# Performance work log

Hardware: AMD Instinct MI355X
Metric: run time of the kernel (lower is better)

The kernel has to match this reference:

```python
import jax, jax.numpy as jnp
import numpy as np


def setup_inputs() -> dict:
    key = jax.random.key(0)
    ks = jax.random.split(key, 5)
    B, Cin, Ch, H, W, K = 8, 64, 64, 128, 128, 3
    fan_in = (Cin + Ch) * K * K
    return {
        "x": jax.random.normal(ks[0], (B, Cin, H, W), jnp.float32),
        "prev_h": jax.random.normal(ks[1], (B, Ch, H, W), jnp.float32),
        "prev_c": jax.random.normal(ks[2], (B, Ch, H, W), jnp.float32),
        "W_gates": jax.random.normal(ks[3], (4 * Ch, Cin + Ch, K, K), jnp.float32) / np.sqrt(fan_in),
        "b_gates": jax.random.normal(ks[4], (4 * Ch,), jnp.float32) * 0.01,
    }


def reference(x, prev_h, prev_c, W_gates, b_gates):
    # ConvLSTM cell: conv over concat(input, prev_h) -> 4 gates -> gating.
    pad = W_gates.shape[-1] // 2
    stacked = jnp.concatenate([x, prev_h], axis=1)  # [B, Cin+Ch, H, W]
    gates = jax.lax.conv_general_dilated(
        stacked, W_gates,
        window_strides=(1, 1),
        padding=[(pad, pad), (pad, pad)],
        dimension_numbers=("NCHW", "OIHW", "NCHW"),
    ) + b_gates[None, :, None, None]  # [B, 4*Ch, H, W]
    in_gate, remember_gate, out_gate, cell_gate = jnp.split(gates, 4, axis=1)
    in_gate = jax.nn.sigmoid(in_gate)
    remember_gate = jax.nn.sigmoid(remember_gate)
    out_gate = jax.nn.sigmoid(out_gate)
    cell_gate = jnp.tanh(cell_gate)
    cell = in_gate * cell_gate + remember_gate * prev_c
    hidden = out_gate * jnp.tanh(cell)
    return (hidden, cell)
```

## Files before the change

### kernel.cpp

```cpp
#include <hip/hip_runtime.h>

typedef __attribute__((ext_vector_type(8))) short short8;
typedef __attribute__((ext_vector_type(16))) float float16;

#define NPIX_HID 8388608

__device__ __forceinline__ short f2bf(float f) {
    union { float f; unsigned u; } v; v.f = f;
    unsigned r = (v.u + 0x7FFFu + ((v.u >> 16) & 1u)) >> 16;
    return (short)r;
}

__device__ __forceinline__ float sigmoidf_(float v) { return 1.f / (1.f + __expf(-v)); }
__device__ __forceinline__ float tanhf_(float v)    { return 2.f / (1.f + __expf(-2.f * v)) - 1.f; }

__global__ void wprep(const float* __restrict__ W, short* __restrict__ A) {
    int tid = blockIdx.x * 256 + threadIdx.x;
    if (tid >= 9 * 16 * 8 * 32 * 8) return;
    int j   = tid & 7;
    int r   = (tid >> 3) & 31;
    int t   = (tid >> 8) & 7;
    int cig = (tid >> 11) & 15;
    int kk  = tid >> 15;
    int g = r >> 3, cl = r & 7;
    int co = g * 64 + t * 8 + cl;
    int ci = cig * 8 + j;
    A[tid] = f2bf(W[co * 1152 + ci * 9 + kk]);
}

__global__ __launch_bounds__(256, 2) void convlstm_main(
    const float* __restrict__ x, const float* __restrict__ ph,
    const float* __restrict__ pc, const short* __restrict__ aprep,
    const float* __restrict__ bg, float* __restrict__ out)
{
    __shared__ short Bs[4 * 66 * 128];

    const int tid  = threadIdx.x;
    const int lane = tid & 63;
    const int wave = tid >> 6;
    const int l31  = lane & 31;
    const int h    = lane >> 5;
    const int mhalf = wave & 1;
    const int nhalf = wave >> 1;

    const int t  = blockIdx.x;
    const int x0 = (t & 1) * 64;
    const int y0 = ((t >> 1) & 63) * 2;
    const int b  = t >> 7;

    for (int i = tid; i < 4224; i += 256) {
        const int px  = i % 66;
        const int ro  = i / 66;
        const int oct = ro & 15;
        const int row = ro >> 4;
        const int ysrc = y0 + row - 1;
        const int xsrc = x0 + px - 1;
        short8 pk = {0,0,0,0,0,0,0,0};
        if ((unsigned)ysrc < 128u && (unsigned)xsrc < 128u) {
            const float* src = (oct < 8) ? x : ph;
            const float* sp = src + (((b * 64 + (oct & 7) * 8) * 128 + ysrc) * 128 + xsrc);
#pragma unroll
            for (int j = 0; j < 8; ++j) pk[j] = f2bf(sp[j * 16384]);
        }
        const int off16 = (row * 66 + px) * 16 + (oct ^ (px & 15));
        *(short8*)&Bs[off16 * 8] = pk;
    }
    __syncthreads();

    float16 acc[4][2];
#pragma unroll
    for (int mt = 0; mt < 4; ++mt)
#pragma unroll
        for (int nt = 0; nt < 2; ++nt)
#pragma unroll
            for (int e = 0; e < 16; ++e) acc[mt][nt][e] = 0.f;

    const short* ap0 = aprep + h * 2048 + l31 * 8 + mhalf * 1024;
    const short* ap1 = ap0 + 4096;

    short8 abuf[2][2][4];
#pragma unroll
    for (int ks = 0; ks < 2; ++ks)
#pragma unroll
        for (int mt = 0; mt < 4; ++mt)
            abuf[0][ks][mt] = *(const short8*)((ks ? ap1 : ap0) + mt * 256);

    const int lB = l31;

#define HALF_BODY(KT, P, ADV)                                                      \
    {                                                                              \
        const int kt  = (KT);                                                      \
        const int kkk = kt >> 2, kc = kt & 3;                                      \
        const int ky  = (kkk * 11) >> 5;                                           \
        const int kx  = kkk - ky * 3;                                              \
        if (ADV) { ap0 += 8192; ap1 += 8192;                                       \
            _Pragma("unroll")                                                      \
            for (int ks = 0; ks < 2; ++ks)                                         \
                _Pragma("unroll")                                                  \
                for (int mt = 0; mt < 4; ++mt)                                     \
                    abuf[(P) ^ 1][ks][mt] =                                        \
                        *(const short8*)((ks ? ap1 : ap0) + mt * 256);             \
        }                                                                          \
        const int pxb = kx + lB;                                                   \
        const int q   = pxb & 15;                                                  \
        const int rh  = ky + nhalf;                                                \
        short8 bfr[2][2];                                                          \
        _Pragma("unroll")                                                          \
        for (int ks = 0; ks < 2; ++ks) {                                           \
            const int gx = ((kc * 4 + ks * 2) | h) ^ q;                            \
            _Pragma("unroll")                                                      \
            for (int nt = 0; nt < 2; ++nt) {                                       \
                const int off16 = (rh * 66 + nt * 32 + pxb) * 16 + gx;             \
                bfr[ks][nt] = *(const short8*)&Bs[off16 * 8];                      \
            }                                                                      \
        }                                                                          \
        _Pragma("unroll")                                                          \
        for (int mt = 0; mt < 4; ++mt)                                             \
            _Pragma("unroll")                                                      \
            for (int nt = 0; nt < 2; ++nt) {                                       \
                acc[mt][nt] = __builtin_amdgcn_mfma_f32_32x32x16_bf16(             \
                    abuf[P][0][mt], bfr[0][nt], acc[mt][nt], 0, 0, 0);             \
                acc[mt][nt] = __builtin_amdgcn_mfma_f32_32x32x16_bf16(             \
                    abuf[P][1][mt], bfr[1][nt], acc[mt][nt], 0, 0, 0);             \
            }                                                                      \
    }

#pragma unroll 1
    for (int it = 0; it < 18; ++it) {
        const int kt0 = it * 2;
        HALF_BODY(kt0, 0, 1)
        HALF_BODY(kt0 + 1, 1, (it < 17))
    }
#undef HALF_BODY

    const int yy = y0 + nhalf;
#pragma unroll
    for (int mt = 0; mt < 4; ++mt) {
        const int c0 = (mhalf * 4 + mt) * 8 + 4 * h;
#pragma unroll
        for (int nt = 0; nt < 2; ++nt) {
            const int px = x0 + nt * 32 + l31;
#pragma unroll
            for (int a = 0; a < 4; ++a) {
                const int c = c0 + a;
                const float gi = acc[mt][nt][a]      + bg[c];
                const float gf = acc[mt][nt][4 + a]  + bg[64 + c];
                const float go = acc[mt][nt][8 + a]  + bg[128 + c];
                const float gc = acc[mt][nt][12 + a] + bg[192 + c];
                const float ig = sigmoidf_(gi);
                const float fg = sigmoidf_(gf);
                const float og = sigmoidf_(go);
                const float cg = tanhf_(gc);
                const int idx = ((b * 64 + c) * 128 + yy) * 128 + px;
                const float cell = ig * cg + fg * pc[idx];
                const float hid  = og * tanhf_(cell);
                out[idx] = hid;
                out[NPIX_HID + idx] = cell;
            }
        }
    }
}

extern "C" void kernel_launch(void* const* d_in, const int* in_sizes, int n_in,
                              void* d_out, int out_size, void* d_ws, size_t ws_size,
                              hipStream_t stream) {
    const float* x  = (const float*)d_in[0];
    const float* ph = (const float*)d_in[1];
    const float* pc = (const float*)d_in[2];
    const float* W  = (const float*)d_in[3];
    const float* bg = (const float*)d_in[4];
    float* out = (float*)d_out;
    short* aprep = (short*)d_ws;

    wprep<<<1152, 256, 0, stream>>>(W, aprep);
    convlstm_main<<<1024, 256, 0, stream>>>(x, ph, pc, aprep, bg, out);
}
```

Measured before the change: 235.0 us.

## Pre-convert inputs to bf16 pixel-major layout and tile conv by full rows

Adds a separate kernel that converts x and prev_h to bf16 in a pixel-major, channel-contiguous layout in workspace. The main kernel then copies contiguous 16-byte vectors into a padded shared-memory buffer instead of doing strided fp32 gathers with inline conversion. Each block now handles one full output row, processes the input channels in two 64-channel phases to keep shared memory small, and uses a matching reordered weight layout. The cost is an extra pass that writes and rereads a 32 MB intermediate plus an extra launch. The old path is kept as a fallback when the workspace is too small.

```diff
diff --git a/kernel.cpp b/kernel.cpp
--- a/kernel.cpp
+++ b/kernel.cpp
@@ -1,39 +1,59 @@
 #include <hip/hip_runtime.h>
 
 typedef __attribute__((ext_vector_type(8))) short short8;
+typedef __attribute__((ext_vector_type(4))) short short4v;
 typedef __attribute__((ext_vector_type(16))) float float16;
 
 #define NPIX_HID 8388608
+#define ROWU 1170
+#define ROWB 18720
+#define WS_NEED (589824u + 33554432u)
 
 __device__ __forceinline__ short f2bf(float f) {
     union { float f; unsigned u; } v; v.f = f;
     unsigned r = (v.u + 0x7FFFu + ((v.u >> 16) & 1u)) >> 16;
     return (short)r;
 }
-
 __device__ __forceinline__ float sigmoidf_(float v) { return 1.f / (1.f + __expf(-v)); }
 __device__ __forceinline__ float tanhf_(float v)    { return 2.f / (1.f + __expf(-2.f * v)) - 1.f; }
 
-__global__ void wprep(const float* __restrict__ W, short* __restrict__ A) {
+__global__ void wprep2(const float* __restrict__ W, short* __restrict__ A) {
     int tid = blockIdx.x * 256 + threadIdx.x;
-    if (tid >= 9 * 16 * 8 * 32 * 8) return;
-    int j   = tid & 7;
-    int r   = (tid >> 3) & 31;
-    int t   = (tid >> 8) & 7;
-    int cig = (tid >> 11) & 15;
-    int kk  = tid >> 15;
-    int g = r >> 3, cl = r & 7;
-    int co = g * 64 + t * 8 + cl;
-    int ci = cig * 8 + j;
-    A[tid] = f2bf(W[co * 1152 + ci * 9 + kk]);
-}
-
-__global__ __launch_bounds__(256, 2) void convlstm_main(
-    const float* __restrict__ x, const float* __restrict__ ph,
-    const float* __restrict__ pc, const short* __restrict__ aprep,
-    const float* __restrict__ bg, float* __restrict__ out)
+    if (tid >= 294912) return;
+    int j = tid & 7, r = (tid >> 3) & 31, t = (tid >> 8) & 7;
+    int h = (tid >> 11) & 1, s = (tid >> 12) & 3;
+    int ht = tid >> 14;
+    int half = ht / 9, tap = ht - half * 9;
+    int co = (r >> 3) * 64 + t * 8 + (r & 7);
+    int ci = half * 64 + s * 16 + h * 8 + j;
+    A[tid] = f2bf(W[co * 1152 + ci * 9 + tap]);
+}
+
+__global__ void bprep_k(const float* __restrict__ x, const float* __restrict__ ph,
+                        short* __restrict__ B) {
+    int tid = blockIdx.x * 256 + threadIdx.x;
+    int px = tid & 127;
+    int yy = (tid >> 7) & 127;
+    int half = (tid >> 14) & 1;
+    int bb = tid >> 15;
+    const float* src = half ? ph : x;
+    const float* sp = src + ((size_t)(bb * 64) * 128 + yy) * 128 + px;
+    short* dst = B + (size_t)(((bb * 128 + yy) * 2 + half)) * 8192 + px * 64;
+#pragma unroll
+    for (int oct = 0; oct < 8; ++oct) {
+        short8 pk;
+#pragma unroll
+        for (int j = 0; j < 8; ++j) pk[j] = f2bf(sp[(oct * 8 + j) * 16384]);
+        *(short8*)(dst + oct * 8) = pk;
+    }
+}
+
+__global__ __launch_bounds__(256, 2) void convlstm_mainB(
+    const short* __restrict__ bprep, const short* __restrict__ aprep,
+    const float* __restrict__ pc, const float* __restrict__ bg,
+    float* __restrict__ out)
 {
-    __shared__ short Bs[4 * 66 * 128];
+    __shared__ short Bs[3 * ROWU * 8];
 
     const int tid  = threadIdx.x;
     const int lane = tid & 63;
@@ -41,20 +61,170 @@
     const int l31  = lane & 31;
     const int h    = lane >> 5;
     const int mhalf = wave & 1;
-    const int nhalf = wave >> 1;
+    const int xhalf = wave >> 1;
 
     const int t  = blockIdx.x;
-    const int x0 = (t & 1) * 64;
-    const int y0 = ((t >> 1) & 63) * 2;
+    const int y0 = t & 127;
     const int b  = t >> 7;
 
+    float16 acc[4][2];
+#pragma unroll
+    for (int mt = 0; mt < 4; ++mt)
+#pragma unroll
+        for (int nt = 0; nt < 2; ++nt)
+#pragma unroll
+            for (int e = 0; e < 16; ++e) acc[mt][nt][e] = 0.f;
+
+    const short* apl = aprep + h * 2048 + mhalf * 1024 + l31 * 8;
+    short8 abuf[2][2][4];
+#pragma unroll
+    for (int ss = 0; ss < 2; ++ss)
+#pragma unroll
+        for (int mt = 0; mt < 4; ++mt)
+            abuf[0][ss][mt] = *(const short8*)(apl + ss * 4096 + mt * 256);
+    const short* apn = apl + 8192;
+
+    const int vb = ((xhalf * 64 + l31) * 9 + h) * 16;
+    char* bsb = (char*)Bs;
+
+#pragma unroll 1
+    for (int phse = 0; phse < 2; ++phse) {
+        if (phse) __syncthreads();
+        if (tid < 48) {
+            int r = tid >> 4, sd = (tid >> 3) & 1, oc = tid & 7;
+            short8 z = {0,0,0,0,0,0,0,0};
+            *(short8*)&Bs[(r * ROWU + sd * 129 * 9 + oc) * 8] = z;
+        }
+#pragma unroll 1
+        for (int r = 0; r < 3; ++r) {
+            int ysrc = y0 + r - 1;
+            if ((unsigned)ysrc < 128u) {
+                const short* gsrc = bprep + (size_t)(((b * 128 + ysrc) * 2 + phse)) * 8192;
+#pragma unroll
+                for (int c = 0; c < 4; ++c) {
+                    int k = c * 256 + tid;
+                    int px = k >> 3, oc = k & 7;
+                    short8 v = *(const short8*)(gsrc + k * 8);
+                    *(short8*)&Bs[(r * ROWU + (px + 1) * 9 + oc) * 8] = v;
+                }
+            } else {
+                short8 z = {0,0,0,0,0,0,0,0};
+#pragma unroll
+                for (int c = 0; c < 4; ++c) {
+                    int k = c * 256 + tid;
+                    int px = k >> 3, oc = k & 7;
+                    *(short8*)&Bs[(r * ROWU + (px + 1) * 9 + oc) * 8] = z;
+                }
+            }
+        }
+        __syncthreads();
+
+#pragma unroll 1
+        for (int q2 = 0; q2 < 9; ++q2) {
+            const int ky = q2 / 3;
+            const int kx = q2 - ky * 3;
+            const int ub = ky * ROWB + kx * 144;
+            {
+#pragma unroll
+                for (int ss = 0; ss < 2; ++ss)
+#pragma unroll
+                    for (int mt = 0; mt < 4; ++mt)
+                        abuf[1][ss][mt] = *(const short8*)(apn + ss * 4096 + mt * 256);
+                apn += 8192;
+#pragma unroll
+                for (int ss = 0; ss < 2; ++ss) {
+                    short8 bfr[2];
+#pragma unroll
+                    for (int nt = 0; nt < 2; ++nt)
+                        bfr[nt] = *(const short8*)(bsb + vb + (ub + nt * 4608 + ss * 32));
+#pragma unroll
+                    for (int mt = 0; mt < 4; ++mt)
+#pragma unroll
+                        for (int nt = 0; nt < 2; ++nt)
+                            acc[mt][nt] = __builtin_amdgcn_mfma_f32_32x32x16_bf16(
+                                abuf[0][ss][mt], bfr[nt], acc[mt][nt], 0, 0, 0);
+                }
+            }
+            {
+                if (!((phse == 1) && (q2 == 8))) {
+#pragma unroll
+                    for (int ss = 0; ss < 2; ++ss)
+#pragma unroll
+                        for (int mt = 0; mt < 4; ++mt)
+                            abuf[0][ss][mt] = *(const short8*)(apn + ss * 4096 + mt * 256);
+                    apn += 8192;
+                }
+#pragma unroll
+                for (int ss = 0; ss < 2; ++ss) {
+                    const int s = 2 + ss;
+                    short8 bfr[2];
+#pragma unroll
+                    for (int nt = 0; nt < 2; ++nt)
+                        bfr[nt] = *(const short8*)(bsb + vb + (ub + nt * 4608 + s * 32));
+#pragma unroll
+                    for (int mt = 0; mt < 4; ++mt)
+#pragma unroll
+                        for (int nt = 0; nt < 2; ++nt)
+                            acc[mt][nt] = __builtin_amdgcn_mfma_f32_32x32x16_bf16(
+                                abuf[1][ss][mt], bfr[nt], acc[mt][nt], 0, 0, 0);
+                }
+            }
+        }
+    }
+
+#pragma unroll
+    for (int mt = 0; mt < 4; ++mt) {
+        const int c0 = (mhalf * 4 + mt) * 8 + 4 * h;
+#pragma unroll
+        for (int nt = 0; nt < 2; ++nt) {
+            const int px = xhalf * 64 + nt * 32 + l31;
+#pragma unroll
+            for (int a = 0; a < 4; ++a) {
+                const int c = c0 + a;
+                const float gi = acc[mt][nt][a]      + bg[c];
+                const float gf = acc[mt][nt][4 + a]  + bg[64 + c];
+                const float go = acc[mt][nt][8 + a]  + bg[128 + c];
+                const float gc = acc[mt][nt][12 + a] + bg[192 + c];
+                const float ig = sigmoidf_(gi);
+                const float fg = sigmoidf_(gf);
+                const float og = sigmoidf_(go);
+                const float cg = tanhf_(gc);
+                const int idx = ((b * 64 + c) * 128 + y0) * 128 + px;
+                const float cell = ig * cg + fg * pc[idx];
+                const float hid  = og * tanhf_(cell);
+                out[idx] = hid;
+                out[NPIX_HID + idx] = cell;
+            }
+        }
+    }
+}
+
+__global__ void wprep5(const float* __restrict__ W, short* __restrict__ A) {
+    int tid = blockIdx.x * 256 + threadIdx.x;
+    if (tid >= 9 * 16 * 8 * 32 * 8) return;
+    int j = tid & 7, r = (tid >> 3) & 31, t = (tid >> 8) & 7;
+    int cig = (tid >> 11) & 15, kk = tid >> 15;
+    int g = r >> 3, cl = r & 7;
+    int co = g * 64 + t * 8 + cl;
+    int ci = cig * 8 + j;
+    A[tid] = f2bf(W[co * 1152 + ci * 9 + kk]);
+}
+
+__global__ __launch_bounds__(256, 2) void convlstm_main5(
+    const float* __restrict__ x, const float* __restrict__ ph,
+    const float* __restrict__ pc, const short* __restrict__ aprep,
+    const float* __restrict__ bg, float* __restrict__ out)
+{
+    __shared__ short Bs[4 * 66 * 128];
+    const int tid = threadIdx.x, lane = tid & 63, wave = tid >> 6;
+    const int l31 = lane & 31, h = lane >> 5;
+    const int mhalf = wave & 1, nhalf = wave >> 1;
+    const int t = blockIdx.x;
+    const int x0 = (t & 1) * 64, y0 = ((t >> 1) & 63) * 2, b = t >> 7;
+
     for (int i = tid; i < 4224; i += 256) {
-        const int px  = i % 66;
-        const int ro  = i / 66;
-        const int oct = ro & 15;
-        const int row = ro >> 4;
-        const int ysrc = y0 + row - 1;
-        const int xsrc = x0 + px - 1;
+        const int px = i % 66, ro = i / 66, oct = ro & 15, row = ro >> 4;
+        const int ysrc = y0 + row - 1, xsrc = x0 + px - 1;
         short8 pk = {0,0,0,0,0,0,0,0};
         if ((unsigned)ysrc < 128u && (unsigned)xsrc < 128u) {
             const float* src = (oct < 8) ? x : ph;
@@ -77,7 +247,6 @@
 
     const short* ap0 = aprep + h * 2048 + l31 * 8 + mhalf * 1024;
     const short* ap1 = ap0 + 4096;
-
     short8 abuf[2][2][4];
 #pragma unroll
     for (int ks = 0; ks < 2; ++ks)
@@ -85,14 +254,12 @@
         for (int mt = 0; mt < 4; ++mt)
             abuf[0][ks][mt] = *(const short8*)((ks ? ap1 : ap0) + mt * 256);
 
-    const int lB = l31;
-
 #define HALF_BODY(KT, P, ADV)                                                      \
     {                                                                              \
-        const int kt  = (KT);                                                      \
+        const int kt = (KT);                                                       \
         const int kkk = kt >> 2, kc = kt & 3;                                      \
-        const int ky  = (kkk * 11) >> 5;                                           \
-        const int kx  = kkk - ky * 3;                                              \
+        const int ky = (kkk * 11) >> 5;                                            \
+        const int kx = kkk - ky * 3;                                               \
         if (ADV) { ap0 += 8192; ap1 += 8192;                                       \
             _Pragma("unroll")                                                      \
             for (int ks = 0; ks < 2; ++ks)                                         \
@@ -101,9 +268,9 @@
                     abuf[(P) ^ 1][ks][mt] =                                        \
                         *(const short8*)((ks ? ap1 : ap0) + mt * 256);             \
         }                                                                          \
-        const int pxb = kx + lB;                                                   \
-        const int q   = pxb & 15;                                                  \
-        const int rh  = ky + nhalf;                                                \
+        const int pxb = kx + l31;                                                  \
+        const int q = pxb & 15;                                                    \
+        const int rh = ky + nhalf;                                                 \
         short8 bfr[2][2];                                                          \
         _Pragma("unroll")                                                          \
         for (int ks = 0; ks < 2; ++ks) {                                           \
@@ -171,7 +338,14 @@
     const float* bg = (const float*)d_in[4];
     float* out = (float*)d_out;
     short* aprep = (short*)d_ws;
-
-    wprep<<<1152, 256, 0, stream>>>(W, aprep);
-    convlstm_main<<<1024, 256, 0, stream>>>(x, ph, pc, aprep, bg, out);
-}
+    short* bprep = (short*)((char*)d_ws + 589824);
+
+    if (ws_size >= (size_t)WS_NEED) {
+        wprep2<<<1152, 256, 0, stream>>>(W, aprep);
+        bprep_k<<<1024, 256, 0, stream>>>(x, ph, bprep);
+        convlstm_mainB<<<1024, 256, 0, stream>>>(bprep, aprep, pc, bg, out);
+    } else {
+        wprep5<<<1152, 256, 0, stream>>>(W, aprep);
+        convlstm_main5<<<1024, 256, 0, stream>>>(x, ph, pc, aprep, bg, out);
+    }
+}
```

After: 248.5 us. 5.8% more time.
